# Kernel optimization log

Measured on AMD Instinct MI355X. Metric: run time of the kernel, lower is better.

Reference implementation:

```python
import jax, jax.numpy as jnp
import numpy as np

N_NODES = 100000
N_GRAPHS = 256
HIDDEN = 64
IN_DIM = 512


def gcn_conv(x, edge_index, W, b, n_nodes):
    """PyG GCNConv: out = D^{-1/2} (A+I) D^{-1/2} (x W) + b."""
    h = x @ W  # [N, H] -- transform first (as PyG does), messages are small
    src = jnp.concatenate([edge_index[0], jnp.arange(n_nodes)])  # add self loops
    dst = jnp.concatenate([edge_index[1], jnp.arange(n_nodes)])
    ones = jnp.ones(src.shape[0], dtype=h.dtype)
    deg = jax.ops.segment_sum(ones, dst, num_segments=n_nodes)
    dinv = jnp.where(deg > 0, jax.lax.rsqrt(deg), 0.0)
    norm = dinv[src] * dinv[dst]  # [E+N]
    msg = h[src] * norm[:, None]  # gather + scale
    out = jax.ops.segment_sum(msg, dst, num_segments=n_nodes)  # scatter-add
    return out + b


def global_mean_pool(x, batch, num_graphs):
    s = jax.ops.segment_sum(x, batch, num_segments=num_graphs)
    cnt = jax.ops.segment_sum(jnp.ones(x.shape[0], dtype=x.dtype), batch,
                              num_segments=num_graphs)
    return s / jnp.maximum(cnt, 1.0)[:, None]


def setup_inputs() -> dict:
    key = jax.random.key(0)
    ks = jax.random.split(key, 9)
    x = jax.random.normal(ks[0], (N_NODES, IN_DIM), dtype=jnp.float32)
    edge_index = jax.random.randint(ks[1], (2, 1600000), 0, N_NODES, dtype=jnp.int64) \
        if jax.config.jax_enable_x64 else jax.random.randint(ks[1], (2, 1600000), 0, N_NODES).astype(jnp.int32)
    batch = jnp.sort(jax.random.randint(ks[2], (N_NODES,), 0, N_GRAPHS))
    sc1 = 1.0 / np.sqrt(IN_DIM)
    sc2 = 1.0 / np.sqrt(HIDDEN)
    W1 = jax.random.uniform(ks[3], (IN_DIM, HIDDEN), minval=-sc1, maxval=sc1, dtype=jnp.float32)
    b1 = jnp.zeros((HIDDEN,), dtype=jnp.float32)
    W2 = jax.random.uniform(ks[4], (HIDDEN, HIDDEN), minval=-sc2, maxval=sc2, dtype=jnp.float32)
    b2 = jnp.zeros((HIDDEN,), dtype=jnp.float32)
    Wfc = jax.random.uniform(ks[5], (HIDDEN, 1), minval=-sc2, maxval=sc2, dtype=jnp.float32)
    bfc = jnp.zeros((1,), dtype=jnp.float32)
    return {"x": x, "edge_index": edge_index, "batch": batch,
            "W1": W1, "b1": b1, "W2": W2, "b2": b2, "Wfc": Wfc, "bfc": bfc}


def reference(x, edge_index, batch, W1, b1, W2, b2, Wfc, bfc):
    n = x.shape[0]
    h = jax.nn.relu(gcn_conv(x, edge_index, W1, b1, n))
    h = jax.nn.relu(gcn_conv(h, edge_index, W2, b2, n))
    g = global_mean_pool(h, batch, N_GRAPHS)  # [G, H]
    out = g @ Wfc + bfc  # [G, 1]
    return out.squeeze(-1)
```

## Files before the change

kernel.cpp:

```cpp
#include <hip/hip_runtime.h>

#define HIDDEN 64
#define IN_DIM 512
#define CAP 4096
#define NB_MAX 1024

typedef short v8s __attribute__((ext_vector_type(8)));
typedef float v4f __attribute__((ext_vector_type(4)));

static __device__ __forceinline__ unsigned short f2bf(float f) {
    unsigned int u = __float_as_uint(f);
    u = (u + 0x7FFF + ((u >> 16) & 1)) >> 16;
    return (unsigned short)u;
}
static __device__ __forceinline__ float bf2f(unsigned short u) {
    return __uint_as_float(((unsigned int)u) << 16);
}
static __device__ __forceinline__ float bflo(unsigned u) { return __uint_as_float(u << 16); }
static __device__ __forceinline__ float bfhi(unsigned u) { return __uint_as_float(u & 0xffff0000u); }

__global__ void k_init(int* cursor, float* gsum, int* gcnt,
                       unsigned short* bufA, unsigned short* bufB, int n_nodes) {
    int i = blockIdx.x * 256 + threadIdx.x;
    if (i < NB_MAX) cursor[i] = 0;
    if (i < 256) { gsum[i] = 0.f; gcnt[i] = 0; }
    if (i < 64) {
        bufA[(size_t)n_nodes * 64 + i] = 0;
        bufB[(size_t)n_nodes * 64 + i] = 0;
    }
}

__launch_bounds__(256)
__global__ void k_bin(const int* __restrict__ src, const int* __restrict__ dst,
                      int* cursor, unsigned* __restrict__ bucket_data, int n_edges) {
    __shared__ unsigned words[4096];
    __shared__ unsigned short binsh[4096];
    __shared__ int hist[NB_MAX];
    __shared__ int base[NB_MAX];
    const int tid = threadIdx.x;
    const int e0 = blockIdx.x * 4096;
    for (int i = tid; i < NB_MAX; i += 256) hist[i] = 0;
    __syncthreads();
    for (int i = tid; i < 4096; i += 256) {
        int e = e0 + i;
        if (e < n_edges) {
            int d = dst[e], s = src[e];
            words[i] = ((unsigned)s << 7) | (unsigned)(d & 127);
            int b = d >> 7;
            binsh[i] = (unsigned short)b;
            atomicAdd(&hist[b], 1);
        } else binsh[i] = 0xFFFFu;
    }
    __syncthreads();
    for (int b = tid; b < NB_MAX; b += 256) {
        int c = hist[b];
        base[b] = c ? atomicAdd(&cursor[b], c) : 0;
        hist[b] = 0;
    }
    __syncthreads();
    for (int i = tid; i < 4096; i += 256) {
        unsigned short b = binsh[i];
        if (b != 0xFFFFu) {
            int slot = atomicAdd(&hist[b], 1);
            int p = base[b] + slot;
            if (p < CAP) bucket_data[(size_t)b * CAP + p] = words[i];
        }
    }
}

__launch_bounds__(256)
__global__ void k_bexc(const int* __restrict__ cursor, int* __restrict__ bucket_base,
                       int* __restrict__ row_start, int n_nodes, int nbuck) {
    __shared__ int wsum[4];
    const int t = threadIdx.x, lane = t & 63, w = t >> 6;
    int v[4], s = 0;
#pragma unroll
    for (int k = 0; k < 4; ++k) {
        int i = t * 4 + k;
        int c = (i < nbuck) ? cursor[i] : 0;
        if (c > CAP) c = CAP;
        v[k] = s; s += c;
    }
    int inc = s;
#pragma unroll
    for (int off = 1; off < 64; off <<= 1) {
        int u = __shfl_up(inc, off, 64);
        if (lane >= off) inc += u;
    }
    if (lane == 63) wsum[w] = inc;
    __syncthreads();
    int cross = 0;
    for (int i = 0; i < w; ++i) cross += wsum[i];
    int b0 = cross + inc - s;
#pragma unroll
    for (int k = 0; k < 4; ++k) {
        int i = t * 4 + k;
        if (i < NB_MAX) bucket_base[i] = b0 + v[k];
    }
    if (t == 255) row_start[n_nodes] = cross + inc;
}

__launch_bounds__(256)
__global__ void k_csr(const unsigned* __restrict__ bucket_data, const int* __restrict__ cursor,
                      const int* __restrict__ bucket_base,
                      int* __restrict__ row_start, int* __restrict__ csr,
                      float* __restrict__ dinv, int n_nodes) {
    __shared__ unsigned words[CAP];
    __shared__ int cnt[128];
    __shared__ int loff[128];
    __shared__ int cur[128];
    __shared__ int w0sum;
    const int tid = threadIdx.x, bin = blockIdx.x, n0 = bin << 7;
    int c = cursor[bin]; if (c > CAP) c = CAP;
    const unsigned* bd = bucket_data + (size_t)bin * CAP;
    for (int i = tid; i < c; i += 256) words[i] = bd[i];
    if (tid < 128) { cnt[tid] = 0; cur[tid] = 0; }
    __syncthreads();
    for (int i = tid; i < c; i += 256) atomicAdd(&cnt[words[i] & 127], 1);
    __syncthreads();
    int val = 0, inc = 0;
    if (tid < 128) {
        const int lane = tid & 63;
        val = cnt[tid];
        inc = val;
#pragma unroll
        for (int off = 1; off < 64; off <<= 1) {
            int u = __shfl_up(inc, off, 64);
            if (lane >= off) inc += u;
        }
        if (tid == 63) w0sum = inc;
    }
    __syncthreads();
    if (tid < 128) {
        int excl = inc - val + ((tid >= 64) ? w0sum : 0);
        loff[tid] = excl;
        int n = n0 + tid;
        if (n < n_nodes) {
            row_start[n] = bucket_base[bin] + excl;
            dinv[n] = rsqrtf((float)(val + 1));
        }
    }
    __syncthreads();
    const int gbase = bucket_base[bin];
    for (int i = tid; i < c; i += 256) {
        unsigned wd = words[i];
        int d = wd & 127;
        int slot = atomicAdd(&cur[d], 1);
        csr[gbase + loff[d] + slot] = (int)(wd & 0xFFFFFF80u);
    }
}

__global__ void k_prep(const float* __restrict__ W1, const float* __restrict__ W2,
                       unsigned short* __restrict__ Wt, unsigned short* __restrict__ Wt2) {
    int idx = blockIdx.x * 256 + threadIdx.x;
    if (idx < HIDDEN * IN_DIM) {
        int n = idx >> 9, k = idx & 511;
        Wt[(size_t)n * 512 + k] = f2bf(W1[(size_t)k * 64 + n]);
    } else {
        int j = idx - HIDDEN * IN_DIM;
        int n = j >> 6, k = j & 63;
        Wt2[(size_t)n * 64 + k] = f2bf(W2[(size_t)k * 64 + n]);
    }
}

__launch_bounds__(256)
__global__ void k_gemm1m(const float* __restrict__ x, const unsigned short* __restrict__ Wt,
                         const float* __restrict__ dinv, unsigned short* __restrict__ s1,
                         int n_nodes) {
    __shared__ __align__(16) unsigned short lX[64 * 136];
    __shared__ __align__(16) unsigned short lW[64 * 136];
    const int tid  = threadIdx.x;
    const int lane = tid & 63;
    const int w    = tid >> 6;
    const int quad = lane >> 4;
    const int m16  = lane & 15;
    const int row0 = blockIdx.x * 64;

    v4f acc[4];
#pragma unroll
    for (int b = 0; b < 4; ++b) acc[b] = (v4f){0.f, 0.f, 0.f, 0.f};

    for (int kc = 0; kc < IN_DIM; kc += 128) {
        __syncthreads();
#pragma unroll
        for (int i = 0; i < 8; ++i) {
            int fidx = tid + i * 256;
            int r  = fidx >> 5;
            int c4 = fidx & 31;
            int gr = row0 + r;
            float4 v = make_float4(0.f, 0.f, 0.f, 0.f);
            if (gr < n_nodes) v = ((const float4*)(x + (size_t)gr * IN_DIM + kc))[c4];
            ushort4 u = make_ushort4(f2bf(v.x), f2bf(v.y), f2bf(v.z), f2bf(v.w));
            *(ushort4*)(lX + r * 136 + c4 * 4) = u;
        }
#pragma unroll
        for (int i = 0; i < 4; ++i) {
            int idx = tid + i * 256;
            int n  = idx >> 4;
            int c8 = idx & 15;
            uint4 u = *(const uint4*)(Wt + (size_t)n * 512 + kc + c8 * 8);
            *(uint4*)(lW + n * 136 + c8 * 8) = u;
        }
        __syncthreads();
#pragma unroll
        for (int kk = 0; kk < 128; kk += 32) {
            v8s a = *(const v8s*)(lX + (w * 16 + m16) * 136 + kk + quad * 8);
#pragma unroll
            for (int b = 0; b < 4; ++b) {
                v8s bb = *(const v8s*)(lW + (b * 16 + m16) * 136 + kk + quad * 8);
                acc[b] = __builtin_amdgcn_mfma_f32_16x16x32_bf16(a, bb, acc[b], 0, 0, 0);
            }
        }
    }
    __syncthreads();
    float* lC = (float*)lX;
#pragma unroll
    for (int b = 0; b < 4; ++b)
#pragma unroll
        for (int r = 0; r < 4; ++r) {
            int rowt = w * 16 + quad * 4 + r;
            lC[rowt * 65 + b * 16 + m16] = acc[b][r];
        }
    __syncthreads();
#pragma unroll
    for (int i = 0; i < 2; ++i) {
        int base = i * 2048 + tid * 8;
        int r = base >> 6;
        int c = base & 63;
        int gr = row0 + r;
        if (gr < n_nodes) {
            float d = dinv[gr];
            const float* p = lC + r * 65 + c;
            unsigned p0 = (unsigned)f2bf(p[0] * d) | ((unsigned)f2bf(p[1] * d) << 16);
            unsigned p1 = (unsigned)f2bf(p[2] * d) | ((unsigned)f2bf(p[3] * d) << 16);
            unsigned p2 = (unsigned)f2bf(p[4] * d) | ((unsigned)f2bf(p[5] * d) << 16);
            unsigned p3 = (unsigned)f2bf(p[6] * d) | ((unsigned)f2bf(p[7] * d) << 16);
            *(uint4*)(s1 + (size_t)gr * 64 + c) = make_uint4(p0, p1, p2, p3);
        }
    }
}

__launch_bounds__(256)
__global__ void k_agg1(const unsigned short* __restrict__ sin, const int* __restrict__ row_start,
                       const int* __restrict__ csr, const float* __restrict__ dinv,
                       float* __restrict__ tout, int n_nodes) {
    const int tid  = threadIdx.x;
    const int lane = tid & 63;
    const int wave = tid >> 6;
    const int g = lane >> 3;
    const int l = lane & 7;
    const int n = (blockIdx.x * 4 + wave) * 8 + g;
    const bool valid = (n < n_nodes);
    const char* sp = (const char*)sin;
    const int SENTB = n_nodes << 7;

    int rs = 0, re = 0;
    if (valid) { rs = row_start[n]; re = row_start[n + 1]; }

    uint4 us = *(const uint4*)(sp + (size_t)(valid ? (n << 7) : SENTB) + l * 16);
    float acc0 = bflo(us.x), acc1 = bfhi(us.x);
    float acc2 = bflo(us.y), acc3 = bfhi(us.y);
    float acc4 = bflo(us.z), acc5 = bfhi(us.z);
    float acc6 = bflo(us.w), acc7 = bfhi(us.w);

    for (int base = rs; base < re; base += 16) {
        int p0 = base + l;
        int p1 = base + 8 + l;
        int a0 = (p0 < re) ? csr[p0] : SENTB;
        int a1 = (p1 < re) ? csr[p1] : SENTB;
#pragma unroll
        for (int j = 0; j < 8; ++j) {
            int ab = __shfl(a0, g * 8 + j, 64);
            uint4 u = *(const uint4*)(sp + (size_t)(unsigned)ab + l * 16);
            acc0 += bflo(u.x); acc1 += bfhi(u.x);
            acc2 += bflo(u.y); acc3 += bfhi(u.y);
            acc4 += bflo(u.z); acc5 += bfhi(u.z);
            acc6 += bflo(u.w); acc7 += bfhi(u.w);
        }
#pragma unroll
        for (int j = 0; j < 8; ++j) {
            int ab = __shfl(a1, g * 8 + j, 64);
            uint4 u = *(const uint4*)(sp + (size_t)(unsigned)ab + l * 16);
            acc0 += bflo(u.x); acc1 += bfhi(u.x);
            acc2 += bflo(u.y); acc3 += bfhi(u.y);
            acc4 += bflo(u.z); acc5 += bfhi(u.z);
            acc6 += bflo(u.w); acc7 += bfhi(u.w);
        }
    }
    if (valid) {
        float d = dinv[n];
        float* op = tout + (size_t)n * HIDDEN + l * 8;
        *(float4*)op       = make_float4(d * acc0, d * acc1, d * acc2, d * acc3);
        *(float4*)(op + 4) = make_float4(d * acc4, d * acc5, d * acc6, d * acc7);
    }
}

__launch_bounds__(256)
__global__ void k_gemm2m(const float* __restrict__ tin, const unsigned short* __restrict__ Wt2,
                         const float* __restrict__ b1, const float* __restrict__ dinv,
                         unsigned short* __restrict__ sout, int n_nodes) {
    __shared__ __align__(16) unsigned short lX[64 * 136];
    __shared__ __align__(16) unsigned short lW[64 * 72];
    const int tid  = threadIdx.x;
    const int lane = tid & 63;
    const int w    = tid >> 6;
    const int quad = lane >> 4;
    const int m16  = lane & 15;
    const int row0 = blockIdx.x * 64;

#pragma unroll
    for (int i = 0; i < 4; ++i) {
        int fidx = tid + i * 256;
        int r  = fidx >> 4;
        int c4 = fidx & 15;
        int gr = row0 + r;
        float4 v = make_float4(0.f, 0.f, 0.f, 0.f);
        if (gr < n_nodes) v = ((const float4*)(tin + (size_t)gr * HIDDEN))[c4];
        float4 bb = ((const float4*)b1)[c4];
        v.x = fmaxf(v.x + bb.x, 0.f);
        v.y = fmaxf(v.y + bb.y, 0.f);
        v.z = fmaxf(v.z + bb.z, 0.f);
        v.w = fmaxf(v.w + bb.w, 0.f);
        ushort4 u = make_ushort4(f2bf(v.x), f2bf(v.y), f2bf(v.z), f2bf(v.w));
        *(ushort4*)(lX + r * 72 + c4 * 4) = u;
    }
#pragma unroll
    for (int i = 0; i < 2; ++i) {
        int idx = tid + i * 256;
        int n  = idx >> 3;
        int c8 = idx & 7;
        uint4 u = *(const uint4*)(Wt2 + (size_t)n * 64 + c8 * 8);
        *(uint4*)(lW + n * 72 + c8 * 8) = u;
    }
    __syncthreads();
    v4f acc[4];
#pragma unroll
    for (int b = 0; b < 4; ++b) acc[b] = (v4f){0.f, 0.f, 0.f, 0.f};
#pragma unroll
    for (int kk = 0; kk < 64; kk += 32) {
        v8s a = *(const v8s*)(lX + (w * 16 + m16) * 72 + kk + quad * 8);
#pragma unroll
        for (int b = 0; b < 4; ++b) {
            v8s bb = *(const v8s*)(lW + (b * 16 + m16) * 72 + kk + quad * 8);
            acc[b] = __builtin_amdgcn_mfma_f32_16x16x32_bf16(a, bb, acc[b], 0, 0, 0);
        }
    }
    __syncthreads();
    float* lC = (float*)lX;
#pragma unroll
    for (int b = 0; b < 4; ++b)
#pragma unroll
        for (int r = 0; r < 4; ++r) {
            int rowt = w * 16 + quad * 4 + r;
            lC[rowt * 65 + b * 16 + m16] = acc[b][r];
        }
    __syncthreads();
#pragma unroll
    for (int i = 0; i < 2; ++i) {
        int base = i * 2048 + tid * 8;
        int r = base >> 6;
        int c = base & 63;
        int gr = row0 + r;
        if (gr < n_nodes) {
            float d = dinv[gr];
            const float* p = lC + r * 65 + c;
            unsigned p0 = (unsigned)f2bf(p[0] * d) | ((unsigned)f2bf(p[1] * d) << 16);
            unsigned p1 = (unsigned)f2bf(p[2] * d) | ((unsigned)f2bf(p[3] * d) << 16);
            unsigned p2 = (unsigned)f2bf(p[4] * d) | ((unsigned)f2bf(p[5] * d) << 16);
            unsigned p3 = (unsigned)f2bf(p[6] * d) | ((unsigned)f2bf(p[7] * d) << 16);
            *(uint4*)(sout + (size_t)gr * 64 + c) = make_uint4(p0, p1, p2, p3);
        }
    }
}

__launch_bounds__(256)
__global__ void k_layer2pool(const unsigned short* __restrict__ sin, const int* __restrict__ row_start,
                             const int* __restrict__ csr, const float* __restrict__ b2,
                             const float* __restrict__ dinv, const float* __restrict__ Wfc,
                             const int* __restrict__ batch,
                             float* gsum, int* gcnt, int n_nodes) {
    __shared__ float lsum[256];
    __shared__ int   lcnt[256];
    const int tid = threadIdx.x;
    lsum[tid] = 0.f; lcnt[tid] = 0;
    __syncthreads();
    const int lane = tid & 63;
    const int wave = tid >> 6;
    const int g = lane >> 3;
    const int l = lane & 7;
    const int n = (blockIdx.x * 4 + wave) * 8 + g;
    const bool valid = (n < n_nodes);
    const char* sp = (const char*)sin;
    const int SENTB = n_nodes << 7;

    int rs = 0, re = 0;
    if (valid) { rs = row_start[n]; re = row_start[n + 1]; }

    uint4 us = *(const uint4*)(sp + (size_t)(valid ? (n << 7) : SENTB) + l * 16);
    float acc0 = bflo(us.x), acc1 = bfhi(us.x);
    float acc2 = bflo(us.y), acc3 = bfhi(us.y);
    float acc4 = bflo(us.z), acc5 = bfhi(us.z);
    float acc6 = bflo(us.w), acc7 = bfhi(us.w);

    for (int base = rs; base < re; base += 16) {
        int p0 = base + l;
        int p1 = base + 8 + l;
        int a0 = (p0 < re) ? csr[p0] : SENTB;
        int a1 = (p1 < re) ? csr[p1] : SENTB;
#pragma unroll
        for (int j = 0; j < 8; ++j) {
            int ab = __shfl(a0, g * 8 + j, 64);
            uint4 u = *(const uint4*)(sp + (size_t)(unsigned)ab + l * 16);
            acc0 += bflo(u.x); acc1 += bfhi(u.x);
            acc2 += bflo(u.y); acc3 += bfhi(u.y);
            acc4 += bflo(u.z); acc5 += bfhi(u.z);
            acc6 += bflo(u.w); acc7 += bfhi(u.w);
        }
#pragma unroll
        for (int j = 0; j < 8; ++j) {
            int ab = __shfl(a1, g * 8 + j, 64);
            uint4 u = *(const uint4*)(sp + (size_t)(unsigned)ab + l * 16);
            acc0 += bflo(u.x); acc1 += bfhi(u.x);
            acc2 += bflo(u.y); acc3 += bfhi(u.y);
            acc4 += bflo(u.z); acc5 += bfhi(u.z);
            acc6 += bflo(u.w); acc7 += bfhi(u.w);
        }
    }
    float d = dinv[valid ? n : 0];
    const float4 bA  = ((const float4*)b2)[2 * l];
    const float4 bB  = ((const float4*)b2)[2 * l + 1];
    const float4 wA  = ((const float4*)Wfc)[2 * l];
    const float4 wB  = ((const float4*)Wfc)[2 * l + 1];
    float t = fmaxf(fmaf(d, acc0, bA.x), 0.f) * wA.x
            + fmaxf(fmaf(d, acc1, bA.y), 0.f) * wA.y
            + fmaxf(fmaf(d, acc2, bA.z), 0.f) * wA.z
            + fmaxf(fmaf(d, acc3, bA.w), 0.f) * wA.w
            + fmaxf(fmaf(d, acc4, bB.x), 0.f) * wB.x
            + fmaxf(fmaf(d, acc5, bB.y), 0.f) * wB.y
            + fmaxf(fmaf(d, acc6, bB.z), 0.f) * wB.z
            + fmaxf(fmaf(d, acc7, bB.w), 0.f) * wB.w;
#pragma unroll
    for (int off = 4; off; off >>= 1) t += __shfl_down(t, off, 8);
    if (l == 0 && valid) {
        int gr = batch[n];
        atomicAdd(&lsum[gr], t);
        atomicAdd(&lcnt[gr], 1);
    }
    __syncthreads();
    if (lcnt[tid]) {
        atomicAdd(&gsum[tid], lsum[tid]);
        atomicAdd(&gcnt[tid], lcnt[tid]);
    }
}

__global__ void k_out(const float* __restrict__ gsum, const int* __restrict__ gcnt,
                      const float* __restrict__ bfc, float* out) {
    int g = threadIdx.x;
    if (g < 256) {
        float c = (float)(gcnt[g] > 1 ? gcnt[g] : 1);
        out[g] = gsum[g] / c + bfc[0];
    }
}

extern "C" void kernel_launch(void* const* d_in, const int* in_sizes, int n_in,
                              void* d_out, int out_size, void* d_ws, size_t ws_size,
                              hipStream_t stream) {
    const float* x   = (const float*)d_in[0];
    const int*   ei  = (const int*)d_in[1];
    const int*   bat = (const int*)d_in[2];
    const float* W1  = (const float*)d_in[3];
    const float* b1  = (const float*)d_in[4];
    const float* W2  = (const float*)d_in[5];
    const float* b2  = (const float*)d_in[6];
    const float* Wfc = (const float*)d_in[7];
    const float* bfc = (const float*)d_in[8];
    float* out = (float*)d_out;

    const int n_nodes = in_sizes[2];
    const int n_edges = in_sizes[1] / 2;
    const int* src = ei;
    const int* dst = ei + n_edges;
    const int NBUCK = (n_nodes + 127) >> 7;

    char* w = (char*)d_ws;
    size_t off = 0;
    auto alloc = [&](size_t bytes) -> void* {
        void* p = w + off;
        off += (bytes + 255) & ~(size_t)255;
        return p;
    };
    float* dinv = (float*)alloc((size_t)n_nodes * sizeof(float));
    unsigned short* bufA = (unsigned short*)alloc(((size_t)n_nodes + 1) * HIDDEN * 2);
    unsigned short* bufB = (unsigned short*)alloc(((size_t)n_nodes + 1) * HIDDEN * 2);
    float* tbuf = (float*)alloc((size_t)n_nodes * HIDDEN * sizeof(float));
    unsigned short* Wt   = (unsigned short*)alloc((size_t)HIDDEN * IN_DIM * 2);
    unsigned short* Wt2  = (unsigned short*)alloc((size_t)HIDDEN * HIDDEN * 2);
    float* gsum = (float*)alloc(256 * sizeof(float));
    int*   gcnt = (int*)  alloc(256 * sizeof(int));
    int*   cursor      = (int*)alloc((size_t)NB_MAX * sizeof(int));
    int*   bucket_base = (int*)alloc((size_t)NB_MAX * sizeof(int));
    unsigned* bucket_data = (unsigned*)alloc((size_t)NB_MAX * CAP * sizeof(unsigned));
    int* row_start = (int*)alloc(((size_t)n_nodes + 1) * sizeof(int));
    int* csr       = (int*)alloc(((size_t)n_edges + 64) * sizeof(int));
    (void)ws_size; (void)n_in; (void)out_size;

    hipLaunchKernelGGL(k_init, dim3(NB_MAX / 256), dim3(256), 0, stream,
                       cursor, gsum, gcnt, bufA, bufB, n_nodes);
    hipLaunchKernelGGL(k_bin, dim3((n_edges + 4095) / 4096), dim3(256), 0, stream,
                       src, dst, cursor, bucket_data, n_edges);
    hipLaunchKernelGGL(k_bexc, dim3(1), dim3(256), 0, stream,
                       cursor, bucket_base, row_start, n_nodes, NBUCK);
    hipLaunchKernelGGL(k_csr, dim3(NBUCK), dim3(256), 0, stream,
                       bucket_data, cursor, bucket_base, row_start, csr, dinv, n_nodes);
    hipLaunchKernelGGL(k_prep, dim3((HIDDEN * IN_DIM + HIDDEN * HIDDEN) / 256), dim3(256), 0, stream,
                       W1, W2, Wt, Wt2);
    hipLaunchKernelGGL(k_gemm1m, dim3((n_nodes + 63) / 64), dim3(256), 0, stream,
                       x, Wt, dinv, bufA, n_nodes);
    const int gb = (n_nodes + 31) / 32;
    hipLaunchKernelGGL(k_agg1, dim3(gb), dim3(256), 0, stream,
                       bufA, row_start, csr, dinv, tbuf, n_nodes);
    hipLaunchKernelGGL(k_gemm2m, dim3((n_nodes + 63) / 64), dim3(256), 0, stream,
                       tbuf, Wt2, b1, dinv, bufB, n_nodes);
    hipLaunchKernelGGL(k_layer2pool, dim3(gb), dim3(256), 0, stream,
                       bufB, row_start, csr, b2, dinv, Wfc, bat, gsum, gcnt, n_nodes);
    hipLaunchKernelGGL(k_out, dim3(1), dim3(256), 0, stream, gsum, gcnt, bfc, out);
}
```

Measured before the change: 422.4 us.

## Fuse layer-1 aggregation with layer-2 GEMM via shared-memory MFMA epilogue

Merges the layer-1 neighbor aggregation kernel with the layer-2 64x64 transform. Each 32-node block aggregates rows, applies bias, ReLU and bf16 conversion, stages them in LDS, then runs MFMA against W2 and writes the dinv-scaled bf16 output. This drops the fp32 intermediate buffer round-trip (about 25.6MB written and then read back) and one kernel launch. In exchange the gather kernel now uses more LDS and ends with barriers and a small GEMM, which may lower occupancy while it is latency-bound on gathers.

```diff
diff --git a/kernel.cpp b/kernel.cpp
--- a/kernel.cpp
+++ b/kernel.cpp
@@ -241,18 +241,32 @@
 }
 
 __launch_bounds__(256)
-__global__ void k_agg1(const unsigned short* __restrict__ sin, const int* __restrict__ row_start,
-                       const int* __restrict__ csr, const float* __restrict__ dinv,
-                       float* __restrict__ tout, int n_nodes) {
+__global__ void k_agg1g2(const unsigned short* __restrict__ sin, const int* __restrict__ row_start,
+                         const int* __restrict__ csr, const float* __restrict__ dinv,
+                         const unsigned short* __restrict__ Wt2, const float* __restrict__ b1,
+                         unsigned short* __restrict__ sout, int n_nodes) {
+    __shared__ __align__(16) unsigned short lW[64 * 72];
+    __shared__ __align__(16) unsigned short lA[32 * 72];
+    __shared__ __align__(16) float lC[32 * 65];
     const int tid  = threadIdx.x;
     const int lane = tid & 63;
     const int wave = tid >> 6;
     const int g = lane >> 3;
     const int l = lane & 7;
-    const int n = (blockIdx.x * 4 + wave) * 8 + g;
+    const int row0 = blockIdx.x * 32;
+    const int n = row0 + wave * 8 + g;
     const bool valid = (n < n_nodes);
     const char* sp = (const char*)sin;
     const int SENTB = n_nodes << 7;
+
+#pragma unroll
+    for (int i = 0; i < 2; ++i) {
+        int idx = tid + i * 256;
+        int nn = idx >> 3;
+        int c8 = idx & 7;
+        uint4 u = *(const uint4*)(Wt2 + (size_t)nn * 64 + c8 * 8);
+        *(uint4*)(lW + nn * 72 + c8 * 8) = u;
+    }
 
     int rs = 0, re = 0;
     if (valid) { rs = row_start[n]; re = row_start[n + 1]; }
@@ -287,77 +301,49 @@
             acc6 += bflo(u.w); acc7 += bfhi(u.w);
         }
     }
-    if (valid) {
-        float d = dinv[n];
-        float* op = tout + (size_t)n * HIDDEN + l * 8;
-        *(float4*)op       = make_float4(d * acc0, d * acc1, d * acc2, d * acc3);
-        *(float4*)(op + 4) = make_float4(d * acc4, d * acc5, d * acc6, d * acc7);
-    }
-}
-
-__launch_bounds__(256)
-__global__ void k_gemm2m(const float* __restrict__ tin, const unsigned short* __restrict__ Wt2,
-                         const float* __restrict__ b1, const float* __restrict__ dinv,
-                         unsigned short* __restrict__ sout, int n_nodes) {
-    __shared__ __align__(16) unsigned short lX[64 * 136];
-    __shared__ __align__(16) unsigned short lW[64 * 72];
-    const int tid  = threadIdx.x;
-    const int lane = tid & 63;
-    const int w    = tid >> 6;
-    const int quad = lane >> 4;
-    const int m16  = lane & 15;
-    const int row0 = blockIdx.x * 64;
-
-#pragma unroll
-    for (int i = 0; i < 4; ++i) {
-        int fidx = tid + i * 256;
-        int r  = fidx >> 4;
-        int c4 = fidx & 15;
-        int gr = row0 + r;
-        float4 v = make_float4(0.f, 0.f, 0.f, 0.f);
-        if (gr < n_nodes) v = ((const float4*)(tin + (size_t)gr * HIDDEN))[c4];
-        float4 bb = ((const float4*)b1)[c4];
-        v.x = fmaxf(v.x + bb.x, 0.f);
-        v.y = fmaxf(v.y + bb.y, 0.f);
-        v.z = fmaxf(v.z + bb.z, 0.f);
-        v.w = fmaxf(v.w + bb.w, 0.f);
-        ushort4 u = make_ushort4(f2bf(v.x), f2bf(v.y), f2bf(v.z), f2bf(v.w));
-        *(ushort4*)(lX + r * 72 + c4 * 4) = u;
-    }
-#pragma unroll
-    for (int i = 0; i < 2; ++i) {
-        int idx = tid + i * 256;
-        int n  = idx >> 3;
-        int c8 = idx & 7;
-        uint4 u = *(const uint4*)(Wt2 + (size_t)n * 64 + c8 * 8);
-        *(uint4*)(lW + n * 72 + c8 * 8) = u;
-    }
-    __syncthreads();
-    v4f acc[4];
-#pragma unroll
-    for (int b = 0; b < 4; ++b) acc[b] = (v4f){0.f, 0.f, 0.f, 0.f};
-#pragma unroll
-    for (int kk = 0; kk < 64; kk += 32) {
-        v8s a = *(const v8s*)(lX + (w * 16 + m16) * 72 + kk + quad * 8);
-#pragma unroll
-        for (int b = 0; b < 4; ++b) {
-            v8s bb = *(const v8s*)(lW + (b * 16 + m16) * 72 + kk + quad * 8);
-            acc[b] = __builtin_amdgcn_mfma_f32_16x16x32_bf16(a, bb, acc[b], 0, 0, 0);
-        }
-    }
-    __syncthreads();
-    float* lC = (float*)lX;
-#pragma unroll
-    for (int b = 0; b < 4; ++b)
+    {
+        float d = valid ? dinv[n] : 0.f;
+        const float4 bA = ((const float4*)b1)[2 * l];
+        const float4 bB = ((const float4*)b1)[2 * l + 1];
+        float t0 = d * acc0, t1 = d * acc1, t2 = d * acc2, t3 = d * acc3;
+        float t4 = d * acc4, t5 = d * acc5, t6 = d * acc6, t7 = d * acc7;
+        float v0 = fmaxf(t0 + bA.x, 0.f), v1 = fmaxf(t1 + bA.y, 0.f);
+        float v2 = fmaxf(t2 + bA.z, 0.f), v3 = fmaxf(t3 + bA.w, 0.f);
+        float v4 = fmaxf(t4 + bB.x, 0.f), v5 = fmaxf(t5 + bB.y, 0.f);
+        float v6 = fmaxf(t6 + bB.z, 0.f), v7 = fmaxf(t7 + bB.w, 0.f);
+        unsigned q0 = (unsigned)f2bf(v0) | ((unsigned)f2bf(v1) << 16);
+        unsigned q1 = (unsigned)f2bf(v2) | ((unsigned)f2bf(v3) << 16);
+        unsigned q2 = (unsigned)f2bf(v4) | ((unsigned)f2bf(v5) << 16);
+        unsigned q3 = (unsigned)f2bf(v6) | ((unsigned)f2bf(v7) << 16);
+        int r = wave * 8 + g;
+        *(uint4*)(lA + r * 72 + l * 8) = make_uint4(q0, q1, q2, q3);
+    }
+    __syncthreads();
+    {
+        const int m16  = lane & 15;
+        const int quad = lane >> 4;
+        const int mt  = wave >> 1;
+        const int nt0 = (wave & 1) * 2;
+        v4f c0 = (v4f){0.f, 0.f, 0.f, 0.f};
+        v4f c1 = (v4f){0.f, 0.f, 0.f, 0.f};
+#pragma unroll
+        for (int kk = 0; kk < 64; kk += 32) {
+            v8s a  = *(const v8s*)(lA + (mt * 16 + m16) * 72 + kk + quad * 8);
+            v8s b0 = *(const v8s*)(lW + (nt0 * 16 + m16) * 72 + kk + quad * 8);
+            v8s b1v = *(const v8s*)(lW + ((nt0 + 1) * 16 + m16) * 72 + kk + quad * 8);
+            c0 = __builtin_amdgcn_mfma_f32_16x16x32_bf16(a, b0, c0, 0, 0, 0);
+            c1 = __builtin_amdgcn_mfma_f32_16x16x32_bf16(a, b1v, c1, 0, 0, 0);
+        }
 #pragma unroll
         for (int r = 0; r < 4; ++r) {
-            int rowt = w * 16 + quad * 4 + r;
-            lC[rowt * 65 + b * 16 + m16] = acc[b][r];
-        }
-    __syncthreads();
-#pragma unroll
-    for (int i = 0; i < 2; ++i) {
-        int base = i * 2048 + tid * 8;
+            int rowt = mt * 16 + quad * 4 + r;
+            lC[rowt * 65 + nt0 * 16 + m16]       = c0[r];
+            lC[rowt * 65 + (nt0 + 1) * 16 + m16] = c1[r];
+        }
+    }
+    __syncthreads();
+    {
+        int base = tid * 8;
         int r = base >> 6;
         int c = base & 63;
         int gr = row0 + r;
@@ -492,7 +478,6 @@
     float* dinv = (float*)alloc((size_t)n_nodes * sizeof(float));
     unsigned short* bufA = (unsigned short*)alloc(((size_t)n_nodes + 1) * HIDDEN * 2);
     unsigned short* bufB = (unsigned short*)alloc(((size_t)n_nodes + 1) * HIDDEN * 2);
-    float* tbuf = (float*)alloc((size_t)n_nodes * HIDDEN * sizeof(float));
     unsigned short* Wt   = (unsigned short*)alloc((size_t)HIDDEN * IN_DIM * 2);
     unsigned short* Wt2  = (unsigned short*)alloc((size_t)HIDDEN * HIDDEN * 2);
     float* gsum = (float*)alloc(256 * sizeof(float));
@@ -516,12 +501,9 @@
                        W1, W2, Wt, Wt2);
     hipLaunchKernelGGL(k_gemm1m, dim3((n_nodes + 63) / 64), dim3(256), 0, stream,
                        x, Wt, dinv, bufA, n_nodes);
-    const int gb = (n_nodes + 31) / 32;
-    hipLaunchKernelGGL(k_agg1, dim3(gb), dim3(256), 0, stream,
-                       bufA, row_start, csr, dinv, tbuf, n_nodes);
-    hipLaunchKernelGGL(k_gemm2m, dim3((n_nodes + 63) / 64), dim3(256), 0, stream,
-                       tbuf, Wt2, b1, dinv, bufB, n_nodes);
-    hipLaunchKernelGGL(k_layer2pool, dim3(gb), dim3(256), 0, stream,
+    hipLaunchKernelGGL(k_agg1g2, dim3((n_nodes + 31) / 32), dim3(256), 0, stream,
+                       bufA, row_start, csr, dinv, Wt2, b1, bufB, n_nodes);
+    hipLaunchKernelGGL(k_layer2pool, dim3((n_nodes + 31) / 32), dim3(256), 0, stream,
                        bufB, row_start, csr, b2, dinv, Wfc, bat, gsum, gcnt, n_nodes);
     hipLaunchKernelGGL(k_out, dim3(1), dim3(256), 0, stream, gsum, gcnt, bfc, out);
 }
```

Result: no change. 415.3 us (-1.7%).
